# Performance work log

Measured on AMD Instinct MI355X. Metric: run time of the kernel, lower is better.

## Reference

```python
import jax, jax.numpy as jnp
import numpy as np
import math

D_MODEL, N_HEADS, D_K, D_C, D_HR = 1024, 8, 128, 32, 32
B, S = 4, 2048


def setup_inputs() -> dict:
    key = jax.random.key(0)
    ks = jax.random.split(key, 17)
    def lin(k, fan_in, fan_out):
        lim = 1.0 / math.sqrt(fan_in)
        kw, kb = jax.random.split(k)
        W = jax.random.uniform(kw, (fan_in, fan_out), jnp.float32, -lim, lim)
        b = jax.random.uniform(kb, (fan_out,), jnp.float32, -lim, lim)
        return W, b
    W_DQ, b_DQ = lin(ks[0], D_MODEL, D_C)
    W_UQ, b_UQ = lin(ks[1], D_C, N_HEADS * D_K)
    W_DKV, b_DKV = lin(ks[2], D_MODEL, D_C)
    W_UK, b_UK = lin(ks[3], D_C, N_HEADS * D_K)
    W_UV, b_UV = lin(ks[4], D_C, N_HEADS * D_K)
    W_QR, b_QR = lin(ks[5], D_C, N_HEADS * D_HR)
    W_KR, b_KR = lin(ks[6], D_MODEL, D_HR)
    W_O, b_O = lin(ks[7], N_HEADS * D_K, D_MODEL)
    h_t = jax.random.normal(ks[8], (B, S, D_MODEL), jnp.float32)
    return {"h_t": h_t,
            "W_DQ": W_DQ, "b_DQ": b_DQ, "W_UQ": W_UQ, "b_UQ": b_UQ,
            "W_DKV": W_DKV, "b_DKV": b_DKV, "W_UK": W_UK, "b_UK": b_UK,
            "W_UV": W_UV, "b_UV": b_UV, "W_QR": W_QR, "b_QR": b_QR,
            "W_KR": W_KR, "b_KR": b_KR, "W_O": W_O, "b_O": b_O}


def reference(h_t, W_DQ, b_DQ, W_UQ, b_UQ, W_DKV, b_DKV, W_UK, b_UK,
              W_UV, b_UV, W_QR, b_QR, W_KR, b_KR, W_O, b_O):
    b, s, _ = h_t.shape
    # low-rank latent projections
    c_q = h_t @ W_DQ + b_DQ                       # [B,S,d_c]
    c_kv = h_t @ W_DKV + b_DKV                    # [B,S,d_c]
    # content heads: [B,H,S,d_k]
    q_c = (c_q @ W_UQ + b_UQ).reshape(b, s, N_HEADS, D_K).transpose(0, 2, 1, 3)
    k_c = (c_kv @ W_UK + b_UK).reshape(b, s, N_HEADS, D_K).transpose(0, 2, 1, 3)
    v_c = (c_kv @ W_UV + b_UV).reshape(b, s, N_HEADS, D_K).transpose(0, 2, 1, 3)
    # rope sub-dims (apply_rope is identity in the source): [B,H,S,d_hR]
    q_r = (c_q @ W_QR + b_QR).reshape(b, s, N_HEADS, D_HR).transpose(0, 2, 1, 3)
    k_r = (h_t @ W_KR + b_KR)[:, None, :, :]      # [B,1,S,d_hR], shared across heads
    k_r = jnp.broadcast_to(k_r, (b, N_HEADS, s, D_HR))
    # concat content + rope dims
    q = jnp.concatenate([q_c, q_r], axis=-1)      # [B,H,S,d_k+d_hR]
    k = jnp.concatenate([k_c, k_r], axis=-1)
    scale = 1.0 / math.sqrt(D_K + D_HR)
    scores = jnp.einsum('bhsd,bhtd->bhst', q, k) * scale
    attn = jax.nn.softmax(scores, axis=-1)
    o = jnp.einsum('bhst,bhtd->bhsd', attn, v_c)  # [B,H,S,d_k]
    o = o.transpose(0, 2, 1, 3).reshape(b, s, N_HEADS * D_K)
    return o @ W_O + b_O
```

## Files before the change

kernel.cpp:

```cpp
#include <hip/hip_runtime.h>
#include <hip/hip_bf16.h>

#define B_SZ 4
#define S_SZ 2048
#define DM   1024
#define NH   8
#define DK   128
#define DC   32
#define DHR  32
#define DQK  160
#define T_TOK (B_SZ * S_SZ)
#define SCALE 0.07905694150420949f
#define C2LOG 0.11405506439f
#define NT    (S_SZ / 64)
#define NCOL  3328

typedef unsigned int uint;
typedef unsigned short ushort;
typedef __attribute__((ext_vector_type(8))) short short8;
typedef __attribute__((ext_vector_type(4))) float floatx4;
typedef __attribute__((ext_vector_type(16))) float floatx16;
typedef __attribute__((ext_vector_type(4))) uint uintx4;

__device__ __forceinline__ ushort f2bf(float f) {
    uint u = __float_as_uint(f);
    uint r = u + 0x7fffu + ((u >> 16) & 1u);
    return (ushort)(r >> 16);
}
__device__ __forceinline__ uint packbf(float x, float y) {
    return (uint)f2bf(x) | ((uint)f2bf(y) << 16);
}

__device__ __forceinline__ void glds16(const ushort* g, ushort* l) {
    __builtin_amdgcn_global_load_lds(
        (const __attribute__((address_space(1))) uint*)g,
        (__attribute__((address_space(3))) uint*)l, 16, 0, 0);
}

__global__ __launch_bounds__(256) void prep_kernel(
    const float* __restrict__ W_O,
    const float* __restrict__ W_UQ, const float* __restrict__ b_UQ,
    const float* __restrict__ W_QR, const float* __restrict__ b_QR,
    const float* __restrict__ W_UK, const float* __restrict__ b_UK,
    const float* __restrict__ W_UV, const float* __restrict__ b_UV,
    const float* __restrict__ W_DQ, const float* __restrict__ b_DQ,
    const float* __restrict__ W_DKV, const float* __restrict__ b_DKV,
    const float* __restrict__ W_KR, const float* __restrict__ b_KR,
    ushort* __restrict__ wot,
    ushort* __restrict__ wcat, float* __restrict__ bcat,
    ushort* __restrict__ wdcat, float* __restrict__ bdcat)
{
    __shared__ float t[32][33];
    const int bid = blockIdx.x;
    const int tx = threadIdx.x & 31, ty = threadIdx.x >> 5;

    if (bid < 1024) {
        const int n0 = (bid & 31) * 32, k0 = (bid >> 5) * 32;
        #pragma unroll
        for (int j = 0; j < 32; j += 8)
            t[ty + j][tx] = W_O[(size_t)(k0 + ty + j) * DM + n0 + tx];
        __syncthreads();
        #pragma unroll
        for (int j = 0; j < 32; j += 8)
            wot[(size_t)(n0 + ty + j) * DM + k0 + tx] = f2bf(t[tx][ty + j]);
    } else if (bid < 1128) {
        const int c0 = (bid - 1024) * 32;
        const float* W; const float* bias; int stride, sc0;
        if (c0 < 1024)      { W = W_UQ; bias = b_UQ; stride = 1024; sc0 = c0; }
        else if (c0 < 1280) { W = W_QR; bias = b_QR; stride = 256;  sc0 = c0 - 1024; }
        else if (c0 < 2304) { W = W_UK; bias = b_UK; stride = 1024; sc0 = c0 - 1280; }
        else                { W = W_UV; bias = b_UV; stride = 1024; sc0 = c0 - 2304; }
        #pragma unroll
        for (int j = 0; j < 4; ++j) {
            int k = ty + j * 8;
            t[k][tx] = W[(size_t)k * stride + sc0 + tx];
        }
        __syncthreads();
        #pragma unroll
        for (int j = 0; j < 4; ++j) {
            int cc = ty + j * 8;
            wcat[(size_t)(c0 + cc) * 32 + tx] = f2bf(t[tx][cc]);
        }
        if (threadIdx.x < 32) bcat[c0 + threadIdx.x] = bias[sc0 + threadIdx.x];
    } else {
        const int idx = bid - 1128;
        const int wsel = idx >> 5;
        const int k0 = (idx & 31) * 32;
        const float* W    = (wsel == 0) ? W_DQ  : (wsel == 1) ? W_DKV : W_KR;
        const float* bias = (wsel == 0) ? b_DQ  : (wsel == 1) ? b_DKV : b_KR;
        #pragma unroll
        for (int j = 0; j < 32; j += 8)
            t[ty + j][tx] = W[(size_t)(k0 + ty + j) * 32 + tx];
        __syncthreads();
        #pragma unroll
        for (int j = 0; j < 32; j += 8)
            wdcat[(size_t)(wsel * 32 + ty + j) * DM + k0 + tx] = f2bf(t[tx][ty + j]);
        if (k0 == 0 && threadIdx.x < 32)
            bdcat[wsel * 32 + threadIdx.x] = bias[threadIdx.x];
    }
}

__global__ __launch_bounds__(128) void latent_mfma_kernel(
    const float* __restrict__ h_t,
    const ushort* __restrict__ wdcat, const float* __restrict__ bdcat,
    ushort* __restrict__ cqbf, ushort* __restrict__ ckvbf, ushort* __restrict__ krbf)
{
    __shared__ __align__(16) float hsl[2 * 2048];
    const int tid  = threadIdx.x;
    const int wave = tid >> 6;
    const int lane = tid & 63;
    const int quad = lane >> 4;
    const int l16  = lane & 15;
    const int t0 = blockIdx.x * 16;

    int soff[4], ldst[4];
    #pragma unroll
    for (int j = 0; j < 4; ++j) {
        int d = (tid + j * 128) * 16;
        int la = d ^ (((d >> 9) & 7) << 4);
        soff[j] = (d >> 9) * 4096 + (la & 511);
        ldst[j] = (wave * 64 + j * 128) * 16;
    }
    const char* hbase = (const char*)(h_t + (size_t)t0 * DM);

    #pragma unroll
    for (int j = 0; j < 4; ++j)
        glds16((const ushort*)(hbase + soff[j]), (ushort*)((char*)hsl + ldst[j]));

    floatx4 acc[3];
    #pragma unroll
    for (int ct = 0; ct < 3; ++ct) acc[ct] = (floatx4){0.f, 0.f, 0.f, 0.f};

    const int xorm = (l16 & 7) << 4;

    for (int c = 0; c < 8; ++c) {
        const int cur = c & 1, nxt = cur ^ 1;
        __syncthreads();
        if (c + 1 < 8) {
            #pragma unroll
            for (int j = 0; j < 4; ++j)
                glds16((const ushort*)(hbase + (c + 1) * 512 + soff[j]),
                       (ushort*)((char*)hsl + nxt * 8192 + ldst[j]));
        }
        const char* hb = (const char*)hsl + cur * 8192;
        #pragma unroll
        for (int st = 0; st < 4; ++st) {
            const int la0 = l16 * 512 + st * 128 + quad * 32;
            float4 f0 = *(const float4*)(hb + (la0 ^ xorm));
            float4 f1 = *(const float4*)(hb + ((la0 + 16) ^ xorm));
            uint b0, b1, b2, b3;
            asm("v_cvt_pk_bf16_f32 %0, %1, %2" : "=v"(b0) : "v"(f0.x), "v"(f0.y));
            asm("v_cvt_pk_bf16_f32 %0, %1, %2" : "=v"(b1) : "v"(f0.z), "v"(f0.w));
            asm("v_cvt_pk_bf16_f32 %0, %1, %2" : "=v"(b2) : "v"(f1.x), "v"(f1.y));
            asm("v_cvt_pk_bf16_f32 %0, %1, %2" : "=v"(b3) : "v"(f1.z), "v"(f1.w));
            short8 bfr = __builtin_bit_cast(short8, (uintx4){b0, b1, b2, b3});
            #pragma unroll
            for (int ct = 0; ct < 3; ++ct) {
                const int wct = wave * 3 + ct;
                short8 af = *(const short8*)&wdcat[(size_t)(wct * 16 + l16) * DM
                                                   + c * 128 + st * 32 + quad * 8];
                acc[ct] = __builtin_amdgcn_mfma_f32_16x16x32_bf16(af, bfr, acc[ct], 0, 0, 0);
            }
        }
    }

    const int q4 = quad * 4;
    const int tok = t0 + l16;
    #pragma unroll
    for (int ct = 0; ct < 3; ++ct) {
        const int col = (wave * 3 + ct) * 16 + q4;
        float4 b4 = *(const float4*)&bdcat[col];
        uint w0, w1;
        asm("v_cvt_pk_bf16_f32 %0, %1, %2" : "=v"(w0)
            : "v"(acc[ct][0] + b4.x), "v"(acc[ct][1] + b4.y));
        asm("v_cvt_pk_bf16_f32 %0, %1, %2" : "=v"(w1)
            : "v"(acc[ct][2] + b4.z), "v"(acc[ct][3] + b4.w));
        ushort* outp = (col < 32) ? cqbf : (col < 64) ? ckvbf : krbf;
        *(uint2*)&outp[(size_t)tok * 32 + (col & 31)] = make_uint2(w0, w1);
    }
}

__global__ __launch_bounds__(256) void build_qkv_mfma_kernel(
    const ushort* __restrict__ cqbf, const ushort* __restrict__ ckvbf,
    const ushort* __restrict__ krbf,
    const ushort* __restrict__ wcat, const float* __restrict__ bcat,
    ushort* __restrict__ q_ws, ushort* __restrict__ k_ws, ushort* __restrict__ v_ws)
{
    const int tid  = threadIdx.x;
    const int wave = tid >> 6;
    const int lane = tid & 63;
    const int quad = lane >> 4;
    const int l16  = lane & 15;

    const int tok = blockIdx.x * 64 + wave * 16 + l16;
    const int hp  = blockIdx.y;
    const int bb  = tok >> 11, s = tok & 2047;

    const short8 bq  = *(const short8*)&cqbf[tok * 32 + quad * 8];
    const short8 bkv = *(const short8*)&ckvbf[tok * 32 + quad * 8];
    const uint4  kr  = *(const uint4*)&((const uint*)krbf)[tok * 16 + quad * 4];

    const int q4 = quad * 4;

    auto emit = [&](int wrow, ushort* outp, int dbase, short8 bfrag) {
        short8 af = *(const short8*)&wcat[(size_t)(wrow + l16) * 32 + quad * 8];
        floatx4 d = __builtin_amdgcn_mfma_f32_16x16x32_bf16(
            af, bfrag, (floatx4){0.f, 0.f, 0.f, 0.f}, 0, 0, 0);
        float4 b4 = *(const float4*)&bcat[wrow + q4];
        uint w0, w1;
        asm("v_cvt_pk_bf16_f32 %0, %1, %2" : "=v"(w0)
            : "v"(d[0] + b4.x), "v"(d[1] + b4.y));
        asm("v_cvt_pk_bf16_f32 %0, %1, %2" : "=v"(w1)
            : "v"(d[2] + b4.z), "v"(d[3] + b4.w));
        *(uint2*)&outp[dbase + q4] = make_uint2(w0, w1);
    };

    #pragma unroll
    for (int hh = 0; hh < 2; ++hh) {
        const int h = hp * 2 + hh;
        ushort* qp = q_ws + ((size_t)(bb * NH + h) * S_SZ + s) * DQK;
        ushort* kp = k_ws + ((size_t)(bb * NH + h) * S_SZ + s) * DQK;
        ushort* vp = v_ws + ((size_t)(bb * NH + h) * S_SZ + s) * DK;

        #pragma unroll
        for (int seg = 0; seg < 8; ++seg) emit(h * 128 + seg * 16, qp, seg * 16, bq);
        #pragma unroll
        for (int seg = 0; seg < 2; ++seg) emit(1024 + h * 32 + seg * 16, qp, 128 + seg * 16, bq);
        #pragma unroll
        for (int seg = 0; seg < 8; ++seg) emit(1280 + h * 128 + seg * 16, kp, seg * 16, bkv);
        #pragma unroll
        for (int seg = 0; seg < 8; ++seg) emit(2304 + h * 128 + seg * 16, vp, seg * 16, bkv);

        *(uint4*)&kp[128 + quad * 8] = kr;
    }
}

__global__ __launch_bounds__(256, 2) void attn_mfma_kernel(
    const ushort* __restrict__ q_ws, const ushort* __restrict__ k_ws,
    const ushort* __restrict__ v_ws, ushort* __restrict__ o_ws)
{
    __shared__ __align__(16) ushort SH[38912];
    const int tid  = threadIdx.x;
    const int wave = tid >> 6;
    const int lane = tid & 63;
    const int l32  = lane & 31;
    const int hi   = lane >> 5;
    const int hi8  = hi * 8;

    const int wg = blockIdx.x;
    const int virt = (wg & 7) * 64 + (wg >> 3);
    const int bh = virt >> 4;
    const int b = bh >> 3, h = bh & 7;
    const int s0 = (virt & 15) * 128;
    const int qrow_base = s0 + wave * 32;

    const ushort* kbase = k_ws + (size_t)bh * S_SZ * DQK;
    const ushort* vbase = v_ws + (size_t)bh * S_SZ * DK;

    int ksrc[5];
    #pragma unroll
    for (int j = 0; j < 5; ++j) {
        int d = (tid + j * 256) * 16;
        int r0 = d / 320;
        int la = d;
        #pragma unroll
        for (int dr = -1; dr <= 1; ++dr) {
            int r = r0 + dr;
            int cand = d ^ ((r & 7) << 4);
            if (cand / 320 == r) la = cand;
        }
        ksrc[j] = la;
    }
    const int kdst_us = (wave * 64) * 8;

    short8 qf[10];
    {
        const ushort* qp = q_ws + ((size_t)bh * S_SZ + qrow_base + l32) * DQK + hi8;
        #pragma unroll
        for (int st = 0; st < 10; ++st)
            qf[st] = *(const short8*)&qp[st * 16];
    }

    floatx16 oa[4];
    #pragma unroll
    for (int vt = 0; vt < 4; ++vt)
        oa[vt] = (floatx16){0.f,0.f,0.f,0.f,0.f,0.f,0.f,0.f,
                            0.f,0.f,0.f,0.f,0.f,0.f,0.f,0.f};

    float m2 = -3.0e38f;
    float l_run = 0.f;

    {
        #pragma unroll
        for (int j = 0; j < 5; ++j)
            glds16((const ushort*)((const char*)kbase + ksrc[j]),
                   SH + kdst_us + j * 2048);
        uint vpa[8], vpb[8];
        const uint* vg = (const uint*)vbase;
        #pragma unroll
        for (int c = 0; c < 8; ++c) {
            int kp = wave * 8 + c;
            vpa[c] = vg[(2 * kp) * 64 + lane];
            vpb[c] = vg[(2 * kp + 1) * 64 + lane];
        }
        uint* vt32 = (uint*)(SH + 20480);
        uint lo[8], hh[8];
        #pragma unroll
        for (int c = 0; c < 8; ++c) {
            lo[c] = (vpa[c] & 0xffffu) | (vpb[c] << 16);
            hh[c] = (vpa[c] >> 16) | (vpb[c] & 0xffff0000u);
        }
        *(uint4*)&vt32[(2 * lane) * 36 + wave * 8]     = make_uint4(lo[0], lo[1], lo[4], lo[5]);
        *(uint4*)&vt32[(2 * lane) * 36 + wave * 8 + 4] = make_uint4(lo[2], lo[3], lo[6], lo[7]);
        *(uint4*)&vt32[(2 * lane + 1) * 36 + wave * 8]     = make_uint4(hh[0], hh[1], hh[4], hh[5]);
        *(uint4*)&vt32[(2 * lane + 1) * 36 + wave * 8 + 4] = make_uint4(hh[2], hh[3], hh[6], hh[7]);
    }

    const int kmask = (l32 & 7) << 4;

    for (int kt = 0; kt < NT; ++kt) {
        const int cur = kt & 1, nxt = cur ^ 1;
        __syncthreads();

        uint vpa[8], vpb[8];
        if (kt + 1 < NT) {
            const char* kg = (const char*)(kbase + (size_t)(kt + 1) * 64 * DQK);
            #pragma unroll
            for (int j = 0; j < 5; ++j)
                glds16((const ushort*)(kg + ksrc[j]),
                       SH + nxt * 10240 + kdst_us + j * 2048);
            const uint* vg = (const uint*)(vbase + (size_t)(kt + 1) * 64 * DK);
            #pragma unroll
            for (int c = 0; c < 8; ++c) {
                int kp = wave * 8 + c;
                vpa[c] = vg[(2 * kp) * 64 + lane];
                vpb[c] = vg[(2 * kp + 1) * 64 + lane];
            }
        }

        const char* kbufc = (const char*)(SH + cur * 10240);
        floatx16 sc[2];
        __builtin_amdgcn_s_setprio(1);
        #pragma unroll
        for (int kb = 0; kb < 2; ++kb) {
            floatx16 acc = (floatx16){0.f,0.f,0.f,0.f,0.f,0.f,0.f,0.f,
                                      0.f,0.f,0.f,0.f,0.f,0.f,0.f,0.f};
            const int row_la = (kb * 32 + l32) * 320 + hi * 16;
            #pragma unroll
            for (int st = 0; st < 10; ++st) {
                short8 kf = *(const short8*)(kbufc + ((row_la + st * 32) ^ kmask));
                acc = __builtin_amdgcn_mfma_f32_32x32x16_bf16(kf, qf[st], acc, 0, 0, 0);
            }
            sc[kb] = acc;
        }
        __builtin_amdgcn_s_setprio(0);

        {
            float tmax = -3.0e38f;
            #pragma unroll
            for (int kb = 0; kb < 2; ++kb)
                #pragma unroll
                for (int r = 0; r < 16; ++r)
                    tmax = fmaxf(tmax, sc[kb][r]);
            tmax *= C2LOG;
            tmax = fmaxf(tmax, __shfl_xor(tmax, 32));

            if (__any(tmax > m2 + 8.0f)) {
                float mnew = fmaxf(m2, tmax);
                float al = __builtin_amdgcn_exp2f(m2 - mnew);
                m2 = mnew;
                l_run *= al;
                #pragma unroll
                for (int vt = 0; vt < 4; ++vt)
                    #pragma unroll
                    for (int r = 0; r < 16; ++r)
                        oa[vt][r] *= al;
            }

            float rsum = 0.f;
            #pragma unroll
            for (int kb = 0; kb < 2; ++kb)
                #pragma unroll
                for (int r = 0; r < 16; ++r) {
                    float p = __builtin_amdgcn_exp2f(__builtin_fmaf(sc[kb][r], C2LOG, -m2));
                    sc[kb][r] = p;
                    rsum += p;
                }
            rsum += __shfl_xor(rsum, 32);
            l_run += rsum;
        }

        const ushort* vtc = SH + 20480 + cur * 9216;
        __builtin_amdgcn_s_setprio(1);
        #pragma unroll
        for (int kb = 0; kb < 2; ++kb) {
            #pragma unroll
            for (int s = 0; s < 2; ++s) {
                uint w0, w1, w2, w3;
                asm("v_cvt_pk_bf16_f32 %0, %1, %2" : "=v"(w0)
                    : "v"(sc[kb][8 * s + 0]), "v"(sc[kb][8 * s + 1]));
                asm("v_cvt_pk_bf16_f32 %0, %1, %2" : "=v"(w1)
                    : "v"(sc[kb][8 * s + 2]), "v"(sc[kb][8 * s + 3]));
                asm("v_cvt_pk_bf16_f32 %0, %1, %2" : "=v"(w2)
                    : "v"(sc[kb][8 * s + 4]), "v"(sc[kb][8 * s + 5]));
                asm("v_cvt_pk_bf16_f32 %0, %1, %2" : "=v"(w3)
                    : "v"(sc[kb][8 * s + 6]), "v"(sc[kb][8 * s + 7]));
                short8 pv = __builtin_bit_cast(short8, (uintx4){w0, w1, w2, w3});
                #pragma unroll
                for (int vt = 0; vt < 4; ++vt) {
                    short8 vf = *(const short8*)&vtc[(size_t)(vt * 32 + l32) * 72
                                                     + kb * 32 + s * 16 + hi8];
                    oa[vt] = __builtin_amdgcn_mfma_f32_32x32x16_bf16(vf, pv, oa[vt], 0, 0, 0);
                }
            }
        }
        __builtin_amdgcn_s_setprio(0);

        if (kt + 1 < NT) {
            uint* vt32 = (uint*)(SH + 20480 + nxt * 9216);
            uint lo[8], hh[8];
            #pragma unroll
            for (int c = 0; c < 8; ++c) {
                lo[c] = (vpa[c] & 0xffffu) | (vpb[c] << 16);
                hh[c] = (vpa[c] >> 16) | (vpb[c] & 0xffff0000u);
            }
            *(uint4*)&vt32[(2 * lane) * 36 + wave * 8]     = make_uint4(lo[0], lo[1], lo[4], lo[5]);
            *(uint4*)&vt32[(2 * lane) * 36 + wave * 8 + 4] = make_uint4(lo[2], lo[3], lo[6], lo[7]);
            *(uint4*)&vt32[(2 * lane + 1) * 36 + wave * 8]     = make_uint4(hh[0], hh[1], hh[4], hh[5]);
            *(uint4*)&vt32[(2 * lane + 1) * 36 + wave * 8 + 4] = make_uint4(hh[2], hh[3], hh[6], hh[7]);
        }
    }

    __syncthreads();
    ushort* ot = SH + wave * (32 * 136);
    uint* ot32 = (uint*)ot;
    {
        float inv = 1.0f / l_run;
        #pragma unroll
        for (int vt = 0; vt < 4; ++vt)
            #pragma unroll
            for (int g = 0; g < 4; ++g) {
                int base = l32 * 68 + vt * 16 + g * 4 + hi * 2;
                ot32[base]     = packbf(oa[vt][g * 4 + 0] * inv, oa[vt][g * 4 + 1] * inv);
                ot32[base + 1] = packbf(oa[vt][g * 4 + 2] * inv, oa[vt][g * 4 + 3] * inv);
            }
    }
    #pragma unroll
    for (int pass = 0; pass < 8; ++pass) {
        int row_in = pass * 4 + (lane >> 4);
        int col8 = (lane & 15) * 8;
        uint4 v = *(const uint4*)&ot[row_in * 136 + col8];
        int srow = qrow_base + row_in;
        *(uint4*)(o_ws + (((size_t)b * S_SZ + srow) * NH + h) * DK + col8) = v;
    }
}

__global__ __launch_bounds__(256) void out_gemm_mfma_kernel(
    const ushort* __restrict__ A,
    const ushort* __restrict__ BT,
    const float* __restrict__ b_O, float* __restrict__ out)
{
    __shared__ __align__(16) ushort As[128 * 64];
    __shared__ __align__(16) ushort Bs[128 * 64];

    const int tid = threadIdx.x;
    const int wave = tid >> 6;
    const int lane = tid & 63;
    const int quad = lane >> 4;
    const int l16 = lane & 15;
    const int wr = wave >> 1, wc = wave & 1;

    const int wg = blockIdx.x;
    const int virt = (wg & 7) * 64 + (wg >> 3);
    const int n0 = (virt & 7) * 128;
    const int m0 = (virt >> 3) * 128;

    int soff[4], ldst[4];
    #pragma unroll
    for (int j = 0; j < 4; ++j) {
        int d = (tid + j * 256) * 16;
        int la = d ^ (((d >> 7) & 7) << 4);
        soff[j] = (d >> 7) * 2048 + (la & 127);
        ldst[j] = (wave * 64 + j * 256) * 16;
    }

    floatx4 acc[4][4];
    #pragma unroll
    for (int mt = 0; mt < 4; ++mt)
        #pragma unroll
        for (int nt = 0; nt < 4; ++nt)
            acc[mt][nt] = (floatx4){0.f, 0.f, 0.f, 0.f};

    const int xorm = (l16 & 7) << 4;

    for (int k0 = 0; k0 < DM; k0 += 64) {
        __syncthreads();
        #pragma unroll
        for (int j = 0; j < 4; ++j) {
            glds16((const ushort*)((const char*)A + (size_t)m0 * 2048 + k0 * 2 + soff[j]),
                   (ushort*)((char*)As + ldst[j]));
            glds16((const ushort*)((const char*)BT + (size_t)n0 * 2048 + k0 * 2 + soff[j]),
                   (ushort*)((char*)Bs + ldst[j]));
        }
        __syncthreads();

        short8 af[4][2], bf[4][2];
        #pragma unroll
        for (int mt = 0; mt < 4; ++mt)
            #pragma unroll
            for (int hh = 0; hh < 2; ++hh) {
                int la_a = (wr * 64 + mt * 16 + l16) * 128 + hh * 64 + quad * 16;
                af[mt][hh] = *(const short8*)((const char*)As + (la_a ^ xorm));
                int la_b = (wc * 64 + mt * 16 + l16) * 128 + hh * 64 + quad * 16;
                bf[mt][hh] = *(const short8*)((const char*)Bs + (la_b ^ xorm));
            }
        #pragma unroll
        for (int mt = 0; mt < 4; ++mt)
            #pragma unroll
            for (int nt = 0; nt < 4; ++nt) {
                acc[mt][nt] = __builtin_amdgcn_mfma_f32_16x16x32_bf16(af[mt][0], bf[nt][0], acc[mt][nt], 0, 0, 0);
                acc[mt][nt] = __builtin_amdgcn_mfma_f32_16x16x32_bf16(af[mt][1], bf[nt][1], acc[mt][nt], 0, 0, 0);
            }
    }

    float bo[4];
    #pragma unroll
    for (int nt = 0; nt < 4; ++nt) bo[nt] = b_O[n0 + wc * 64 + nt * 16 + l16];

    #pragma unroll
    for (int mt = 0; mt < 4; ++mt) {
        #pragma unroll
        for (int r = 0; r < 4; ++r) {
            int row = m0 + wr * 64 + mt * 16 + quad * 4 + r;
            float* orow = out + (size_t)row * DM + n0 + wc * 64;
            #pragma unroll
            for (int nt = 0; nt < 4; ++nt)
                orow[nt * 16 + l16] = acc[mt][nt][r] + bo[nt];
        }
    }
}

extern "C" void kernel_launch(void* const* d_in, const int* in_sizes, int n_in,
                              void* d_out, int out_size, void* d_ws, size_t ws_size,
                              hipStream_t stream) {
    (void)in_sizes; (void)n_in; (void)out_size; (void)ws_size;

    const float* h_t   = (const float*)d_in[0];
    const float* W_DQ  = (const float*)d_in[1];
    const float* b_DQ  = (const float*)d_in[2];
    const float* W_UQ  = (const float*)d_in[3];
    const float* b_UQ  = (const float*)d_in[4];
    const float* W_DKV = (const float*)d_in[5];
    const float* b_DKV = (const float*)d_in[6];
    const float* W_UK  = (const float*)d_in[7];
    const float* b_UK  = (const float*)d_in[8];
    const float* W_UV  = (const float*)d_in[9];
    const float* b_UV  = (const float*)d_in[10];
    const float* W_QR  = (const float*)d_in[11];
    const float* b_QR  = (const float*)d_in[12];
    const float* W_KR  = (const float*)d_in[13];
    const float* b_KR  = (const float*)d_in[14];
    const float* W_O   = (const float*)d_in[15];
    const float* b_O   = (const float*)d_in[16];

    ushort* cqbf  = (ushort*)d_ws;
    ushort* ckvbf = cqbf + (size_t)T_TOK * DC;
    ushort* krbf  = ckvbf + (size_t)T_TOK * DC;
    ushort* wcat  = krbf + (size_t)T_TOK * DC;
    float*  bcat  = (float*)(wcat + (size_t)NCOL * DC);
    ushort* wdcat = (ushort*)(bcat + NCOL);
    float*  bdcat = (float*)(wdcat + (size_t)96 * DM);
    ushort* q_ws  = (ushort*)(bdcat + 96);
    ushort* k_ws  = q_ws + (size_t)B_SZ * NH * S_SZ * DQK;
    ushort* v_ws  = k_ws + (size_t)B_SZ * NH * S_SZ * DQK;
    ushort* o_ws  = v_ws + (size_t)B_SZ * NH * S_SZ * DK;
    ushort* wot   = o_ws + (size_t)T_TOK * DM;

    float* out = (float*)d_out;

    prep_kernel<<<1224, 256, 0, stream>>>(
        W_O, W_UQ, b_UQ, W_QR, b_QR, W_UK, b_UK, W_UV, b_UV,
        W_DQ, b_DQ, W_DKV, b_DKV, W_KR, b_KR,
        wot, wcat, bcat, wdcat, bdcat);

    latent_mfma_kernel<<<T_TOK / 16, 128, 0, stream>>>(
        h_t, wdcat, bdcat, cqbf, ckvbf, krbf);

    build_qkv_mfma_kernel<<<dim3(T_TOK / 64, 4), 256, 0, stream>>>(
        cqbf, ckvbf, krbf, wcat, bcat, q_ws, k_ws, v_ws);

    attn_mfma_kernel<<<512, 256, 0, stream>>>(
        q_ws, k_ws, v_ws, o_ws);

    out_gemm_mfma_kernel<<<512, 256, 0, stream>>>(
        o_ws, wot, b_O, out);
}
```

Measured before the change: 271.4 us.

## Double attention block to 8 waves sharing each K/V tile load

The attention kernel now runs 512-thread blocks that each cover 256 query rows instead of 128, so the launch uses half as many blocks. Each K/V tile staged in shared memory is split across 8 waves and reused by twice as many query rows, cutting global K/V traffic per query row. The V transpose buffer is repacked with a narrower row stride to fit. The launch bound changes to (512, 4), which demands much higher occupancy and may cap registers low enough to force spills of the accumulator and Q fragments.

```diff
diff --git a/kernel.cpp b/kernel.cpp
--- a/kernel.cpp
+++ b/kernel.cpp
@@ -235,11 +235,11 @@
     }
 }
 
-__global__ __launch_bounds__(256, 2) void attn_mfma_kernel(
+__global__ __launch_bounds__(512, 4) void attn_mfma_kernel(
     const ushort* __restrict__ q_ws, const ushort* __restrict__ k_ws,
     const ushort* __restrict__ v_ws, ushort* __restrict__ o_ws)
 {
-    __shared__ __align__(16) ushort SH[38912];
+    __shared__ __align__(16) ushort SH[37888];
     const int tid  = threadIdx.x;
     const int wave = tid >> 6;
     const int lane = tid & 63;
@@ -248,19 +248,20 @@
     const int hi8  = hi * 8;
 
     const int wg = blockIdx.x;
-    const int virt = (wg & 7) * 64 + (wg >> 3);
-    const int bh = virt >> 4;
+    const int virt = (wg & 7) * 32 + (wg >> 3);
+    const int bh = virt >> 3;
     const int b = bh >> 3, h = bh & 7;
-    const int s0 = (virt & 15) * 128;
+    const int s0 = (virt & 7) * 256;
     const int qrow_base = s0 + wave * 32;
 
     const ushort* kbase = k_ws + (size_t)bh * S_SZ * DQK;
     const ushort* vbase = v_ws + (size_t)bh * S_SZ * DK;
 
-    int ksrc[5];
-    #pragma unroll
-    for (int j = 0; j < 5; ++j) {
-        int d = (tid + j * 256) * 16;
+    int ksrc[3];
+    const int kch[3] = {wave, wave + 8, wave + 16};
+    #pragma unroll
+    for (int j = 0; j < 3; ++j) {
+        int d = (kch[j] * 64 + lane) * 16;
         int r0 = d / 320;
         int la = d;
         #pragma unroll
@@ -271,7 +272,10 @@
         }
         ksrc[j] = la;
     }
-    const int kdst_us = (wave * 64) * 8;
+
+    const int W8 = (wave >> 1) * 8, vo = wave & 1;
+    const int colA = W8 + (vo ? 2 : 0);
+    const int colB = W8 + (vo ? 6 : 4);
 
     short8 qf[10];
     {
@@ -291,29 +295,29 @@
     float l_run = 0.f;
 
     {
-        #pragma unroll
-        for (int j = 0; j < 5; ++j)
-            glds16((const ushort*)((const char*)kbase + ksrc[j]),
-                   SH + kdst_us + j * 2048);
-        uint vpa[8], vpb[8];
+        glds16((const ushort*)((const char*)kbase + ksrc[0]), SH + kch[0] * 512);
+        glds16((const ushort*)((const char*)kbase + ksrc[1]), SH + kch[1] * 512);
+        if (wave < 4)
+            glds16((const ushort*)((const char*)kbase + ksrc[2]), SH + kch[2] * 512);
+        uint vpa[4], vpb[4];
         const uint* vg = (const uint*)vbase;
         #pragma unroll
-        for (int c = 0; c < 8; ++c) {
-            int kp = wave * 8 + c;
+        for (int c = 0; c < 4; ++c) {
+            int kp = wave * 4 + c;
             vpa[c] = vg[(2 * kp) * 64 + lane];
             vpb[c] = vg[(2 * kp + 1) * 64 + lane];
         }
         uint* vt32 = (uint*)(SH + 20480);
-        uint lo[8], hh[8];
-        #pragma unroll
-        for (int c = 0; c < 8; ++c) {
+        uint lo[4], hh[4];
+        #pragma unroll
+        for (int c = 0; c < 4; ++c) {
             lo[c] = (vpa[c] & 0xffffu) | (vpb[c] << 16);
             hh[c] = (vpa[c] >> 16) | (vpb[c] & 0xffff0000u);
         }
-        *(uint4*)&vt32[(2 * lane) * 36 + wave * 8]     = make_uint4(lo[0], lo[1], lo[4], lo[5]);
-        *(uint4*)&vt32[(2 * lane) * 36 + wave * 8 + 4] = make_uint4(lo[2], lo[3], lo[6], lo[7]);
-        *(uint4*)&vt32[(2 * lane + 1) * 36 + wave * 8]     = make_uint4(hh[0], hh[1], hh[4], hh[5]);
-        *(uint4*)&vt32[(2 * lane + 1) * 36 + wave * 8 + 4] = make_uint4(hh[2], hh[3], hh[6], hh[7]);
+        *(uint2*)&vt32[(2 * lane) * 34 + colA]     = make_uint2(lo[0], lo[1]);
+        *(uint2*)&vt32[(2 * lane) * 34 + colB]     = make_uint2(lo[2], lo[3]);
+        *(uint2*)&vt32[(2 * lane + 1) * 34 + colA] = make_uint2(hh[0], hh[1]);
+        *(uint2*)&vt32[(2 * lane + 1) * 34 + colB] = make_uint2(hh[2], hh[3]);
     }
 
     const int kmask = (l32 & 7) << 4;
@@ -322,17 +326,18 @@
         const int cur = kt & 1, nxt = cur ^ 1;
         __syncthreads();
 
-        uint vpa[8], vpb[8];
+        uint vpa[4], vpb[4];
         if (kt + 1 < NT) {
             const char* kg = (const char*)(kbase + (size_t)(kt + 1) * 64 * DQK);
-            #pragma unroll
-            for (int j = 0; j < 5; ++j)
-                glds16((const ushort*)(kg + ksrc[j]),
-                       SH + nxt * 10240 + kdst_us + j * 2048);
+            ushort* kd = SH + nxt * 10240;
+            glds16((const ushort*)(kg + ksrc[0]), kd + kch[0] * 512);
+            glds16((const ushort*)(kg + ksrc[1]), kd + kch[1] * 512);
+            if (wave < 4)
+                glds16((const ushort*)(kg + ksrc[2]), kd + kch[2] * 512);
             const uint* vg = (const uint*)(vbase + (size_t)(kt + 1) * 64 * DK);
             #pragma unroll
-            for (int c = 0; c < 8; ++c) {
-                int kp = wave * 8 + c;
+            for (int c = 0; c < 4; ++c) {
+                int kp = wave * 4 + c;
                 vpa[c] = vg[(2 * kp) * 64 + lane];
                 vpb[c] = vg[(2 * kp + 1) * 64 + lane];
             }
@@ -390,7 +395,7 @@
             l_run += rsum;
         }
 
-        const ushort* vtc = SH + 20480 + cur * 9216;
+        const ushort* vtc = SH + 20480 + cur * 8704;
         __builtin_amdgcn_s_setprio(1);
         #pragma unroll
         for (int kb = 0; kb < 2; ++kb) {
@@ -408,7 +413,7 @@
                 short8 pv = __builtin_bit_cast(short8, (uintx4){w0, w1, w2, w3});
                 #pragma unroll
                 for (int vt = 0; vt < 4; ++vt) {
-                    short8 vf = *(const short8*)&vtc[(size_t)(vt * 32 + l32) * 72
+                    short8 vf = *(const short8*)&vtc[(size_t)(vt * 32 + l32) * 68
                                                      + kb * 32 + s * 16 + hi8];
                     oa[vt] = __builtin_amdgcn_mfma_f32_32x32x16_bf16(vf, pv, oa[vt], 0, 0, 0);
                 }
@@ -417,17 +422,17 @@
         __builtin_amdgcn_s_setprio(0);
 
         if (kt + 1 < NT) {
-            uint* vt32 = (uint*)(SH + 20480 + nxt * 9216);
-            uint lo[8], hh[8];
-            #pragma unroll
-            for (int c = 0; c < 8; ++c) {
+            uint* vt32 = (uint*)(SH + 20480 + nxt * 8704);
+            uint lo[4], hh[4];
+            #pragma unroll
+            for (int c = 0; c < 4; ++c) {
                 lo[c] = (vpa[c] & 0xffffu) | (vpb[c] << 16);
                 hh[c] = (vpa[c] >> 16) | (vpb[c] & 0xffff0000u);
             }
-            *(uint4*)&vt32[(2 * lane) * 36 + wave * 8]     = make_uint4(lo[0], lo[1], lo[4], lo[5]);
-            *(uint4*)&vt32[(2 * lane) * 36 + wave * 8 + 4] = make_uint4(lo[2], lo[3], lo[6], lo[7]);
-            *(uint4*)&vt32[(2 * lane + 1) * 36 + wave * 8]     = make_uint4(hh[0], hh[1], hh[4], hh[5]);
-            *(uint4*)&vt32[(2 * lane + 1) * 36 + wave * 8 + 4] = make_uint4(hh[2], hh[3], hh[6], hh[7]);
+            *(uint2*)&vt32[(2 * lane) * 34 + colA]     = make_uint2(lo[0], lo[1]);
+            *(uint2*)&vt32[(2 * lane) * 34 + colB]     = make_uint2(lo[2], lo[3]);
+            *(uint2*)&vt32[(2 * lane + 1) * 34 + colA] = make_uint2(hh[0], hh[1]);
+            *(uint2*)&vt32[(2 * lane + 1) * 34 + colB] = make_uint2(hh[2], hh[3]);
         }
     }
 
@@ -589,7 +594,7 @@
     build_qkv_mfma_kernel<<<dim3(T_TOK / 64, 4), 256, 0, stream>>>(
         cqbf, ckvbf, krbf, wcat, bcat, q_ws, k_ws, v_ws);
 
-    attn_mfma_kernel<<<512, 256, 0, stream>>>(
+    attn_mfma_kernel<<<256, 512, 0, stream>>>(
         q_ws, k_ws, v_ws, o_ws);
 
     out_gemm_mfma_kernel<<<512, 256, 0, stream>>>(
```

New measurement: 772.6 us. 185% more time.

## Absorb W_UV into W_O so attention aggregates the latent c_kv directly

Applied to the files above, without the earlier changes.

Attention now multiplies probabilities by the 32-wide latent c_kv per head instead of the 128-wide per-head V. W_UV is folded into W_O with a new precompute kernel that builds a 256x1024 combined weight and a fused bias. This cuts V materialisation, attention PV MFMAs by 4x, LDS usage and the output GEMM K dimension from 1024 to 256. In exchange it adds a small weight-fusion kernel with a naive fp32 bias loop, and P@c_kv runs in bf16 before the up-projection, which may shift rounding.

```diff
diff --git a/kernel.cpp b/kernel.cpp
--- a/kernel.cpp
+++ b/kernel.cpp
@@ -38,7 +38,6 @@
 }
 
 __global__ __launch_bounds__(256) void prep_kernel(
-    const float* __restrict__ W_O,
     const float* __restrict__ W_UQ, const float* __restrict__ b_UQ,
     const float* __restrict__ W_QR, const float* __restrict__ b_QR,
     const float* __restrict__ W_UK, const float* __restrict__ b_UK,
@@ -46,7 +45,6 @@
     const float* __restrict__ W_DQ, const float* __restrict__ b_DQ,
     const float* __restrict__ W_DKV, const float* __restrict__ b_DKV,
     const float* __restrict__ W_KR, const float* __restrict__ b_KR,
-    ushort* __restrict__ wot,
     ushort* __restrict__ wcat, float* __restrict__ bcat,
     ushort* __restrict__ wdcat, float* __restrict__ bdcat)
 {
@@ -54,17 +52,8 @@
     const int bid = blockIdx.x;
     const int tx = threadIdx.x & 31, ty = threadIdx.x >> 5;
 
-    if (bid < 1024) {
-        const int n0 = (bid & 31) * 32, k0 = (bid >> 5) * 32;
-        #pragma unroll
-        for (int j = 0; j < 32; j += 8)
-            t[ty + j][tx] = W_O[(size_t)(k0 + ty + j) * DM + n0 + tx];
-        __syncthreads();
-        #pragma unroll
-        for (int j = 0; j < 32; j += 8)
-            wot[(size_t)(n0 + ty + j) * DM + k0 + tx] = f2bf(t[tx][ty + j]);
-    } else if (bid < 1128) {
-        const int c0 = (bid - 1024) * 32;
+    if (bid < 104) {
+        const int c0 = bid * 32;
         const float* W; const float* bias; int stride, sc0;
         if (c0 < 1024)      { W = W_UQ; bias = b_UQ; stride = 1024; sc0 = c0; }
         else if (c0 < 1280) { W = W_QR; bias = b_QR; stride = 256;  sc0 = c0 - 1024; }
@@ -83,7 +72,7 @@
         }
         if (threadIdx.x < 32) bcat[c0 + threadIdx.x] = bias[sc0 + threadIdx.x];
     } else {
-        const int idx = bid - 1128;
+        const int idx = bid - 104;
         const int wsel = idx >> 5;
         const int k0 = (idx & 31) * 32;
         const float* W    = (wsel == 0) ? W_DQ  : (wsel == 1) ? W_DKV : W_KR;
@@ -97,6 +86,45 @@
             wdcat[(size_t)(wsel * 32 + ty + j) * DM + k0 + tx] = f2bf(t[tx][ty + j]);
         if (k0 == 0 && threadIdx.x < 32)
             bdcat[wsel * 32 + threadIdx.x] = bias[threadIdx.x];
+    }
+}
+
+__global__ __launch_bounds__(256) void wuvo_kernel(
+    const float* __restrict__ W_UV, const float* __restrict__ b_UV,
+    const float* __restrict__ W_O, const float* __restrict__ b_O,
+    ushort* __restrict__ w2t, float* __restrict__ b2)
+{
+    __shared__ float WO[128][64];
+    __shared__ float WUV[32][129];
+    const int bid = blockIdx.x;
+    if (bid < 128) {
+        const int h = bid >> 4, n0 = (bid & 15) * 64;
+        for (int idx = threadIdx.x; idx < 8192; idx += 256) {
+            int r = idx >> 6, c = idx & 63;
+            WO[r][c] = W_O[(size_t)(h * 128 + r) * DM + n0 + c];
+        }
+        for (int idx = threadIdx.x; idx < 4096; idx += 256) {
+            int r = idx >> 7, c = idx & 127;
+            WUV[r][c] = W_UV[(size_t)r * DM + h * 128 + c];
+        }
+        __syncthreads();
+        const int i = threadIdx.x & 31, g = threadIdx.x >> 5;
+        float acc[8] = {0.f, 0.f, 0.f, 0.f, 0.f, 0.f, 0.f, 0.f};
+        for (int j = 0; j < 128; ++j) {
+            float wv = WUV[i][j];
+            #pragma unroll
+            for (int u = 0; u < 8; ++u)
+                acc[u] += wv * WO[j][g * 8 + u];
+        }
+        #pragma unroll
+        for (int u = 0; u < 8; ++u)
+            w2t[(size_t)(n0 + g * 8 + u) * 256 + h * 32 + i] = f2bf(acc[u]);
+    } else {
+        const int n = (bid - 128) * 256 + threadIdx.x;
+        float acc = b_O[n];
+        for (int m = 0; m < 1024; ++m)
+            acc += b_UV[m] * W_O[(size_t)m * DM + n];
+        b2[n] = acc;
     }
 }
 
@@ -148,12 +176,12 @@
             const int la0 = l16 * 512 + st * 128 + quad * 32;
             float4 f0 = *(const float4*)(hb + (la0 ^ xorm));
             float4 f1 = *(const float4*)(hb + ((la0 + 16) ^ xorm));
-            uint b0, b1, b2, b3;
+            uint b0, b1, b2x, b3;
             asm("v_cvt_pk_bf16_f32 %0, %1, %2" : "=v"(b0) : "v"(f0.x), "v"(f0.y));
             asm("v_cvt_pk_bf16_f32 %0, %1, %2" : "=v"(b1) : "v"(f0.z), "v"(f0.w));
-            asm("v_cvt_pk_bf16_f32 %0, %1, %2" : "=v"(b2) : "v"(f1.x), "v"(f1.y));
+            asm("v_cvt_pk_bf16_f32 %0, %1, %2" : "=v"(b2x) : "v"(f1.x), "v"(f1.y));
             asm("v_cvt_pk_bf16_f32 %0, %1, %2" : "=v"(b3) : "v"(f1.z), "v"(f1.w));
-            short8 bfr = __builtin_bit_cast(short8, (uintx4){b0, b1, b2, b3});
+            short8 bfr = __builtin_bit_cast(short8, (uintx4){b0, b1, b2x, b3});
             #pragma unroll
             for (int ct = 0; ct < 3; ++ct) {
                 const int wct = wave * 3 + ct;
@@ -184,7 +212,7 @@
     const ushort* __restrict__ cqbf, const ushort* __restrict__ ckvbf,
     const ushort* __restrict__ krbf,
     const ushort* __restrict__ wcat, const float* __restrict__ bcat,
-    ushort* __restrict__ q_ws, ushort* __restrict__ k_ws, ushort* __restrict__ v_ws)
+    ushort* __restrict__ q_ws, ushort* __restrict__ k_ws)
 {
     const int tid  = threadIdx.x;
     const int wave = tid >> 6;
@@ -220,7 +248,6 @@
         const int h = hp * 2 + hh;
         ushort* qp = q_ws + ((size_t)(bb * NH + h) * S_SZ + s) * DQK;
         ushort* kp = k_ws + ((size_t)(bb * NH + h) * S_SZ + s) * DQK;
-        ushort* vp = v_ws + ((size_t)(bb * NH + h) * S_SZ + s) * DK;
 
         #pragma unroll
         for (int seg = 0; seg < 8; ++seg) emit(h * 128 + seg * 16, qp, seg * 16, bq);
@@ -228,8 +255,6 @@
         for (int seg = 0; seg < 2; ++seg) emit(1024 + h * 32 + seg * 16, qp, 128 + seg * 16, bq);
         #pragma unroll
         for (int seg = 0; seg < 8; ++seg) emit(1280 + h * 128 + seg * 16, kp, seg * 16, bkv);
-        #pragma unroll
-        for (int seg = 0; seg < 8; ++seg) emit(2304 + h * 128 + seg * 16, vp, seg * 16, bkv);
 
         *(uint4*)&kp[128 + quad * 8] = kr;
     }
@@ -237,9 +262,9 @@
 
 __global__ __launch_bounds__(256, 2) void attn_mfma_kernel(
     const ushort* __restrict__ q_ws, const ushort* __restrict__ k_ws,
-    const ushort* __restrict__ v_ws, ushort* __restrict__ o_ws)
+    const ushort* __restrict__ ckvbf, ushort* __restrict__ o2)
 {
-    __shared__ __align__(16) ushort SH[38912];
+    __shared__ __align__(16) ushort SH[24576];
     const int tid  = threadIdx.x;
     const int wave = tid >> 6;
     const int lane = tid & 63;
@@ -255,7 +280,7 @@
     const int qrow_base = s0 + wave * 32;
 
     const ushort* kbase = k_ws + (size_t)bh * S_SZ * DQK;
-    const ushort* vbase = v_ws + (size_t)bh * S_SZ * DK;
+    const uint* cbase = (const uint*)(ckvbf + (size_t)b * S_SZ * DC);
 
     int ksrc[5];
     #pragma unroll
@@ -281,42 +306,44 @@
             qf[st] = *(const short8*)&qp[st * 16];
     }
 
-    floatx16 oa[4];
-    #pragma unroll
-    for (int vt = 0; vt < 4; ++vt)
-        oa[vt] = (floatx16){0.f,0.f,0.f,0.f,0.f,0.f,0.f,0.f,
-                            0.f,0.f,0.f,0.f,0.f,0.f,0.f,0.f};
+    floatx16 oa;
+    oa = (floatx16){0.f,0.f,0.f,0.f,0.f,0.f,0.f,0.f,
+                    0.f,0.f,0.f,0.f,0.f,0.f,0.f,0.f};
 
     float m2 = -3.0e38f;
     float l_run = 0.f;
+
+    const int kmask = (l32 & 7) << 4;
+
 
     {
         #pragma unroll
         for (int j = 0; j < 5; ++j)
             glds16((const ushort*)((const char*)kbase + ksrc[j]),
                    SH + kdst_us + j * 2048);
-        uint vpa[8], vpb[8];
-        const uint* vg = (const uint*)vbase;
-        #pragma unroll
-        for (int c = 0; c < 8; ++c) {
-            int kp = wave * 8 + c;
-            vpa[c] = vg[(2 * kp) * 64 + lane];
-            vpb[c] = vg[(2 * kp + 1) * 64 + lane];
-        }
-        uint* vt32 = (uint*)(SH + 20480);
-        uint lo[8], hh[8];
-        #pragma unroll
-        for (int c = 0; c < 8; ++c) {
-            lo[c] = (vpa[c] & 0xffffu) | (vpb[c] << 16);
-            hh[c] = (vpa[c] >> 16) | (vpb[c] & 0xffff0000u);
-        }
-        *(uint4*)&vt32[(2 * lane) * 36 + wave * 8]     = make_uint4(lo[0], lo[1], lo[4], lo[5]);
-        *(uint4*)&vt32[(2 * lane) * 36 + wave * 8 + 4] = make_uint4(lo[2], lo[3], lo[6], lo[7]);
-        *(uint4*)&vt32[(2 * lane + 1) * 36 + wave * 8]     = make_uint4(hh[0], hh[1], hh[4], hh[5]);
-        *(uint4*)&vt32[(2 * lane + 1) * 36 + wave * 8 + 4] = make_uint4(hh[2], hh[3], hh[6], hh[7]);
-    }
-
-    const int kmask = (l32 & 7) << 4;
+        if (lane < 16) {
+            uint vpa[8], vpb[8];
+            #pragma unroll
+            for (int c = 0; c < 8; ++c) {
+                int kp = wave * 8 + c;
+                vpa[c] = cbase[(2 * kp) * 16 + lane];
+                vpb[c] = cbase[(2 * kp + 1) * 16 + lane];
+            }
+            uint lo[8], hh[8];
+            #pragma unroll
+            for (int c = 0; c < 8; ++c) {
+                lo[c] = (vpa[c] & 0xffffu) | (vpb[c] << 16);
+                hh[c] = (vpa[c] >> 16) | (vpb[c] & 0xffff0000u);
+            }
+            char* base = (char*)(SH + 20480);
+            const int r0 = 2 * lane, r1 = 2 * lane + 1;
+            const int sw0 = (r0 & 7) << 4, sw1 = (r1 & 7) << 4;
+            *(uint4*)(base + ((r0 * 128 + wave * 32) ^ sw0))      = make_uint4(lo[0], lo[1], lo[4], lo[5]);
+            *(uint4*)(base + ((r0 * 128 + wave * 32 + 16) ^ sw0)) = make_uint4(lo[2], lo[3], lo[6], lo[7]);
+            *(uint4*)(base + ((r1 * 128 + wave * 32) ^ sw1))      = make_uint4(hh[0], hh[1], hh[4], hh[5]);
+            *(uint4*)(base + ((r1 * 128 + wave * 32 + 16) ^ sw1)) = make_uint4(hh[2], hh[3], hh[6], hh[7]);
+        }
+    }
 
     for (int kt = 0; kt < NT; ++kt) {
         const int cur = kt & 1, nxt = cur ^ 1;
@@ -329,12 +356,14 @@
             for (int j = 0; j < 5; ++j)
                 glds16((const ushort*)(kg + ksrc[j]),
                        SH + nxt * 10240 + kdst_us + j * 2048);
-            const uint* vg = (const uint*)(vbase + (size_t)(kt + 1) * 64 * DK);
-            #pragma unroll
-            for (int c = 0; c < 8; ++c) {
-                int kp = wave * 8 + c;
-                vpa[c] = vg[(2 * kp) * 64 + lane];
-                vpb[c] = vg[(2 * kp + 1) * 64 + lane];
+            if (lane < 16) {
+                const uint* cg = cbase + (size_t)(kt + 1) * 64 * 16;
+                #pragma unroll
+                for (int c = 0; c < 8; ++c) {
+                    int kp = wave * 8 + c;
+                    vpa[c] = cg[(2 * kp) * 16 + lane];
+                    vpb[c] = cg[(2 * kp + 1) * 16 + lane];
+                }
             }
         }
 
@@ -371,10 +400,8 @@
                 m2 = mnew;
                 l_run *= al;
                 #pragma unroll
-                for (int vt = 0; vt < 4; ++vt)
-                    #pragma unroll
-                    for (int r = 0; r < 16; ++r)
-                        oa[vt][r] *= al;
+                for (int r = 0; r < 16; ++r)
+                    oa[r] *= al;
             }
 
             float rsum = 0.f;
@@ -390,7 +417,7 @@
             l_run += rsum;
         }
 
-        const ushort* vtc = SH + 20480 + cur * 9216;
+        const char* ctc = (const char*)(SH + 20480 + cur * 2048);
         __builtin_amdgcn_s_setprio(1);
         #pragma unroll
         for (int kb = 0; kb < 2; ++kb) {
@@ -406,59 +433,46 @@
                 asm("v_cvt_pk_bf16_f32 %0, %1, %2" : "=v"(w3)
                     : "v"(sc[kb][8 * s + 6]), "v"(sc[kb][8 * s + 7]));
                 short8 pv = __builtin_bit_cast(short8, (uintx4){w0, w1, w2, w3});
-                #pragma unroll
-                for (int vt = 0; vt < 4; ++vt) {
-                    short8 vf = *(const short8*)&vtc[(size_t)(vt * 32 + l32) * 72
-                                                     + kb * 32 + s * 16 + hi8];
-                    oa[vt] = __builtin_amdgcn_mfma_f32_32x32x16_bf16(vf, pv, oa[vt], 0, 0, 0);
-                }
+                const int la = l32 * 128 + kb * 64 + s * 32 + hi * 16;
+                short8 cf = *(const short8*)(ctc + (la ^ kmask));
+                oa = __builtin_amdgcn_mfma_f32_32x32x16_bf16(cf, pv, oa, 0, 0, 0);
             }
         }
         __builtin_amdgcn_s_setprio(0);
 
-        if (kt + 1 < NT) {
-            uint* vt32 = (uint*)(SH + 20480 + nxt * 9216);
+        if (kt + 1 < NT && lane < 16) {
             uint lo[8], hh[8];
             #pragma unroll
             for (int c = 0; c < 8; ++c) {
                 lo[c] = (vpa[c] & 0xffffu) | (vpb[c] << 16);
                 hh[c] = (vpa[c] >> 16) | (vpb[c] & 0xffff0000u);
             }
-            *(uint4*)&vt32[(2 * lane) * 36 + wave * 8]     = make_uint4(lo[0], lo[1], lo[4], lo[5]);
-            *(uint4*)&vt32[(2 * lane) * 36 + wave * 8 + 4] = make_uint4(lo[2], lo[3], lo[6], lo[7]);
-            *(uint4*)&vt32[(2 * lane + 1) * 36 + wave * 8]     = make_uint4(hh[0], hh[1], hh[4], hh[5]);
-            *(uint4*)&vt32[(2 * lane + 1) * 36 + wave * 8 + 4] = make_uint4(hh[2], hh[3], hh[6], hh[7]);
-        }
-    }
-
-    __syncthreads();
-    ushort* ot = SH + wave * (32 * 136);
-    uint* ot32 = (uint*)ot;
+            char* base = (char*)(SH + 20480 + nxt * 2048);
+            const int r0 = 2 * lane, r1 = 2 * lane + 1;
+            const int sw0 = (r0 & 7) << 4, sw1 = (r1 & 7) << 4;
+            *(uint4*)(base + ((r0 * 128 + wave * 32) ^ sw0))      = make_uint4(lo[0], lo[1], lo[4], lo[5]);
+            *(uint4*)(base + ((r0 * 128 + wave * 32 + 16) ^ sw0)) = make_uint4(lo[2], lo[3], lo[6], lo[7]);
+            *(uint4*)(base + ((r1 * 128 + wave * 32) ^ sw1))      = make_uint4(hh[0], hh[1], hh[4], hh[5]);
+            *(uint4*)(base + ((r1 * 128 + wave * 32 + 16) ^ sw1)) = make_uint4(hh[2], hh[3], hh[6], hh[7]);
+        }
+    }
+
     {
         float inv = 1.0f / l_run;
-        #pragma unroll
-        for (int vt = 0; vt < 4; ++vt)
-            #pragma unroll
-            for (int g = 0; g < 4; ++g) {
-                int base = l32 * 68 + vt * 16 + g * 4 + hi * 2;
-                ot32[base]     = packbf(oa[vt][g * 4 + 0] * inv, oa[vt][g * 4 + 1] * inv);
-                ot32[base + 1] = packbf(oa[vt][g * 4 + 2] * inv, oa[vt][g * 4 + 3] * inv);
-            }
-    }
-    #pragma unroll
-    for (int pass = 0; pass < 8; ++pass) {
-        int row_in = pass * 4 + (lane >> 4);
-        int col8 = (lane & 15) * 8;
-        uint4 v = *(const uint4*)&ot[row_in * 136 + col8];
-        int srow = qrow_base + row_in;
-        *(uint4*)(o_ws + (((size_t)b * S_SZ + srow) * NH + h) * DK + col8) = v;
+        ushort* orow = o2 + ((size_t)(b * S_SZ + qrow_base + l32)) * 256 + h * 32 + hi * 4;
+        #pragma unroll
+        for (int g = 0; g < 4; ++g) {
+            uint w0 = packbf(oa[4 * g + 0] * inv, oa[4 * g + 1] * inv);
+            uint w1 = packbf(oa[4 * g + 2] * inv, oa[4 * g + 3] * inv);
+            *(uint2*)&orow[g * 8] = make_uint2(w0, w1);
+        }
     }
 }
 
 __global__ __launch_bounds__(256) void out_gemm_mfma_kernel(
     const ushort* __restrict__ A,
     const ushort* __restrict__ BT,
-    const float* __restrict__ b_O, float* __restrict__ out)
+    const float* __restrict__ b2, float* __restrict__ out)
 {
     __shared__ __align__(16) ushort As[128 * 64];
     __shared__ __align__(16) ushort Bs[128 * 64];
@@ -480,7 +494,7 @@
     for (int j = 0; j < 4; ++j) {
         int d = (tid + j * 256) * 16;
         int la = d ^ (((d >> 7) & 7) << 4);
-        soff[j] = (d >> 7) * 2048 + (la & 127);
+        soff[j] = (d >> 7) * 512 + (la & 127);
         ldst[j] = (wave * 64 + j * 256) * 16;
     }
 
@@ -493,13 +507,13 @@
 
     const int xorm = (l16 & 7) << 4;
 
-    for (int k0 = 0; k0 < DM; k0 += 64) {
+    for (int k0 = 0; k0 < 256; k0 += 64) {
         __syncthreads();
         #pragma unroll
         for (int j = 0; j < 4; ++j) {
-            glds16((const ushort*)((const char*)A + (size_t)m0 * 2048 + k0 * 2 + soff[j]),
+            glds16((const ushort*)((const char*)A + (size_t)m0 * 512 + k0 * 2 + soff[j]),
                    (ushort*)((char*)As + ldst[j]));
-            glds16((const ushort*)((const char*)BT + (size_t)n0 * 2048 + k0 * 2 + soff[j]),
+            glds16((const ushort*)((const char*)BT + (size_t)n0 * 512 + k0 * 2 + soff[j]),
                    (ushort*)((char*)Bs + ldst[j]));
         }
         __syncthreads();
@@ -525,7 +539,7 @@
 
     float bo[4];
     #pragma unroll
-    for (int nt = 0; nt < 4; ++nt) bo[nt] = b_O[n0 + wc * 64 + nt * 16 + l16];
+    for (int nt = 0; nt < 4; ++nt) bo[nt] = b2[n0 + wc * 64 + nt * 16 + l16];
 
     #pragma unroll
     for (int mt = 0; mt < 4; ++mt) {
@@ -572,26 +586,29 @@
     float*  bdcat = (float*)(wdcat + (size_t)96 * DM);
     ushort* q_ws  = (ushort*)(bdcat + 96);
     ushort* k_ws  = q_ws + (size_t)B_SZ * NH * S_SZ * DQK;
-    ushort* v_ws  = k_ws + (size_t)B_SZ * NH * S_SZ * DQK;
-    ushort* o_ws  = v_ws + (size_t)B_SZ * NH * S_SZ * DK;
-    ushort* wot   = o_ws + (size_t)T_TOK * DM;
+    ushort* o2    = k_ws + (size_t)B_SZ * NH * S_SZ * DQK;
+    ushort* w2t   = o2 + (size_t)T_TOK * 256;
+    float*  b2    = (float*)(w2t + (size_t)DM * 256);
 
     float* out = (float*)d_out;
 
-    prep_kernel<<<1224, 256, 0, stream>>>(
-        W_O, W_UQ, b_UQ, W_QR, b_QR, W_UK, b_UK, W_UV, b_UV,
+    prep_kernel<<<200, 256, 0, stream>>>(
+        W_UQ, b_UQ, W_QR, b_QR, W_UK, b_UK, W_UV, b_UV,
         W_DQ, b_DQ, W_DKV, b_DKV, W_KR, b_KR,
-        wot, wcat, bcat, wdcat, bdcat);
+        wcat, bcat, wdcat, bdcat);
+
+    wuvo_kernel<<<132, 256, 0, stream>>>(
+        W_UV, b_UV, W_O, b_O, w2t, b2);
 
     latent_mfma_kernel<<<T_TOK / 16, 128, 0, stream>>>(
         h_t, wdcat, bdcat, cqbf, ckvbf, krbf);
 
     build_qkv_mfma_kernel<<<dim3(T_TOK / 64, 4), 256, 0, stream>>>(
-        cqbf, ckvbf, krbf, wcat, bcat, q_ws, k_ws, v_ws);
+        cqbf, ckvbf, krbf, wcat, bcat, q_ws, k_ws);
 
     attn_mfma_kernel<<<512, 256, 0, stream>>>(
-        q_ws, k_ws, v_ws, o_ws);
+        q_ws, k_ws, ckvbf, o2);
 
     out_gemm_mfma_kernel<<<512, 256, 0, stream>>>(
-        o_ws, wot, b_O, out);
-}
+        o2, w2t, b2, out);
+}
```

Result: faster. 262.1 us (-3.4%).
